# Kernel optimization log

Hardware: AMD Instinct MI355X
Metric: run time of the kernel (lower is better)

The kernel has to match this reference:

```python
import jax, jax.numpy as jnp
import numpy as np

LMAX, MMAX = 4, 2
L = (LMAX + 1) ** 2  # 25 full SH coefficients
_midx = np.concatenate([l * l + l + np.arange(-min(l, MMAX), min(l, MMAX) + 1) for l in range(LMAX + 1)])
M = len(_midx)  # 19 m-restricted coefficients (|m|<=mmax)
_l_of = np.concatenate([np.full(2 * l + 1, l) for l in range(LMAX + 1)])
MIDX = jnp.asarray(_midx)
L_OF = jnp.asarray(_l_of)
LMAP = jnp.asarray((_l_of[:, None] == np.arange(LMAX + 1)[None, :]).astype(np.float32))  # [L, lmax+1]
COUNTS = jnp.asarray((2 * np.arange(LMAX + 1) + 1).astype(np.float32))
AVG_DEGREE = 23.395238876342773
AVG_NUM_NODES = 77.81317
N_NODES, N_EDGES, N_GRAPH = 2500, 50000, 16
C, H, A, VC, FF, NB, NL = 128, 8, 64, 16, 128, 600, 4
MAX_R = 12.0

def rms_norm_sh(x, scale):
    # per-degree-l RMS norm with learned per-(l, channel) scale; x [N,L,C]
    ms = jnp.einsum('nlc,lk->nk', x * x, LMAP) / (COUNTS * x.shape[-1])
    inv = jax.lax.rsqrt(ms + 1e-8)[:, L_OF]  # [N,L]
    return x * inv[..., None] * scale[L_OF][None]

def seg_softmax(logits, seg, n):
    m = jax.ops.segment_max(logits, seg, num_segments=n)
    e = jnp.exp(logits - m[seg])
    s = jax.ops.segment_sum(e, seg, num_segments=n)
    return e / (s[seg] + 1e-9)

def _forward(edge_distance, sphere_emb, W_e1, W_e2, W_deg, norm_scale, norm_scale2,
             Wq, Wk, alpha_vec, Wv, W_rad, Wo, W1, W2, norm_scale_final, W_ef1, W_ef2,
             atomic_numbers, edge_index, batch):
    src, tgt = edge_index[0], edge_index[1]
    # GaussianSmearing(0, max_radius, 600, basis_width_scalar=2.0)
    offset = jnp.linspace(0.0, MAX_R, NB)
    coeff = -0.5 / (2.0 * (MAX_R / (NB - 1))) ** 2
    smear = jnp.exp(coeff * (edge_distance[:, None] - offset[None, :]) ** 2)  # [E,NB]
    efeat = jax.nn.silu(jax.nn.silu(smear @ W_e1) @ W_e2)  # shared radial edge features [E,C]
    # sphere embedding into l=0 coefficient
    x = jnp.zeros((N_NODES, L, C), edge_distance.dtype)
    x = x.at[:, 0, :].set(sphere_emb[atomic_numbers])
    # edge degree embedding: per-edge coefficients scattered to target nodes
    deg = (efeat @ W_deg).reshape(N_EDGES, M, C)
    x = x.at[:, MIDX, :].add(jax.ops.segment_sum(deg, tgt, num_segments=N_NODES) / AVG_DEGREE)
    for i in range(NL):
        # --- SO2 equivariant graph attention ---
        xn = rms_norm_sh(x, norm_scale[i])
        s = xn[:, 0, :]  # invariant (l=0) features [N,C]
        q = (s @ Wq[i]).reshape(N_NODES, H, A)[tgt]
        k = (s @ Wk[i]).reshape(N_NODES, H, A)[src]
        logits = jnp.einsum('eha,ha->eh', jax.nn.silu(q + k), alpha_vec[i]) / np.sqrt(A).astype(np.float32)
        attn = seg_softmax(logits, tgt, N_NODES)  # [E,H]
        rad = jax.nn.silu(efeat @ W_rad[i])  # per-edge per-coefficient radial gate [E,M]
        xm = xn[:, MIDX, :][src] * rad[..., None]  # gather m-restricted coeffs [E,M,C]
        v = jnp.einsum('emc,cd->emd', xm, Wv[i]).reshape(N_EDGES, M, H, VC)
        msg = (v * attn[:, None, :, None]).reshape(N_EDGES, M, H * VC)
        out = jnp.einsum('emd,dc->emc', msg, Wo[i])
        x = x.at[:, MIDX, :].add(jax.ops.segment_sum(out, tgt, num_segments=N_NODES))
        # --- FFN with separable S2 (scalar-gated) activation ---
        xn = rms_norm_sh(x, norm_scale2[i])
        h = jnp.einsum('nlc,cf->nlf', xn, W1[i])
        h = h * jax.nn.silu(h[:, :1, :])
        x = x + jnp.einsum('nlf,fc->nlc', h, W2[i])
    # energy head
    xn = rms_norm_sh(x, norm_scale_final)
    h = jnp.einsum('nlc,cf->nlf', xn, W_ef1)
    h = h * jax.nn.silu(h[:, :1, :])
    node_e = jnp.einsum('nlf,fo->nlo', h, W_ef2)[:, 0, 0]  # l=0 scalar per node
    return jax.ops.segment_sum(node_e, batch, num_segments=N_GRAPH) / AVG_NUM_NODES

def setup_inputs() -> dict:
    key = jax.random.key(0)
    ks = jax.random.split(key, 24)
    rn = lambda k, shp, fan: jax.random.normal(k, shp, jnp.float32) / np.sqrt(fan).astype(np.float32)
    inp = {}
    inp['atomic_numbers'] = jax.random.randint(ks[0], (N_NODES,), 0, 90)
    inp['edge_index'] = jax.random.randint(ks[1], (2, N_EDGES), 0, N_NODES)
    inp['edge_distance'] = jax.random.uniform(ks[2], (N_EDGES,), jnp.float32) * MAX_R
    inp['batch'] = jnp.sort(jax.random.randint(ks[3], (N_NODES,), 0, N_GRAPH))
    inp['sphere_emb'] = rn(ks[4], (90, C), 1)
    inp['W_e1'] = rn(ks[5], (NB, C), NB)
    inp['W_e2'] = rn(ks[6], (C, C), C)
    inp['W_deg'] = rn(ks[7], (C, M * C), C)
    inp['norm_scale'] = jnp.ones((NL, LMAX + 1, C), jnp.float32)
    inp['norm_scale2'] = jnp.ones((NL, LMAX + 1, C), jnp.float32)
    inp['Wq'] = rn(ks[8], (NL, C, H * A), C)
    inp['Wk'] = rn(ks[9], (NL, C, H * A), C)
    inp['alpha_vec'] = rn(ks[10], (NL, H, A), A)
    inp['Wv'] = rn(ks[11], (NL, C, H * VC), C)
    inp['W_rad'] = rn(ks[12], (NL, C, M), C)
    inp['Wo'] = rn(ks[13], (NL, H * VC, C), H * VC)
    inp['W1'] = rn(ks[14], (NL, C, FF), C)
    inp['W2'] = rn(ks[15], (NL, FF, C), FF)
    inp['norm_scale_final'] = jnp.ones((LMAX + 1, C), jnp.float32)
    inp['W_ef1'] = rn(ks[16], (C, FF), C)
    inp['W_ef2'] = rn(ks[17], (FF, 1), FF)
    return inp

def reference(atomic_numbers, edge_index, edge_distance, batch, sphere_emb, W_e1, W_e2, W_deg,
              norm_scale, norm_scale2, Wq, Wk, alpha_vec, Wv, W_rad, Wo, W1, W2,
              norm_scale_final, W_ef1, W_ef2):
    return _forward(edge_distance, sphere_emb, W_e1, W_e2, W_deg, norm_scale, norm_scale2,
                    Wq, Wk, alpha_vec, Wv, W_rad, Wo, W1, W2, norm_scale_final, W_ef1, W_ef2,
                    atomic_numbers, edge_index, batch)
```

## Files before the change

### kernel.cpp

```cpp
#include <hip/hip_runtime.h>
#include <hip/hip_bf16.h>

#define N_NODES 2500
#define N_EDGES 50000
#define C 128
#define MC 19
#define RSTR 20
#define NL 4
#define NB 600
#define GW 10
#define NTAP (2*GW+1)
#define NBUK 4
#define BUKW 625
#define N4 (N_NODES*NBUK)
#define ASTR 136
#define MSTR 132
#define MAXE 96
#define EB 64
#define NQKB ((N_NODES+31)/32)
#define NRADB ((N_EDGES+EB-1)/EB)

typedef float floatx2 __attribute__((ext_vector_type(2)));
typedef short bf16x8 __attribute__((ext_vector_type(8)));
typedef float f32x4 __attribute__((ext_vector_type(4)));
// ... 289 lines not shown
      float2 xv[MC];
      float pl[5]={0.f,0.f,0.f,0.f,0.f};
      #pragma unroll
      for (int m=0;m<MC;m++){
        float2 v = *(const float2*)&x[(size_t)n*MC*C + m*C + lane*2];
        xv[m]=v;
        pl[l_of_m(m)] += v.x*v.x + v.y*v.y;
      }
      #pragma unroll
      for (int l=0;l<5;l++){
        float r = pl[l];
        #pragma unroll
        for (int d=32; d>0; d>>=1) r += __shfl_xor(r, d, 64);
        pl[l]=r;
      }
      const float dens[5] = {128.f,384.f,640.f,896.f,1152.f};
      float inv[5];
      #pragma unroll
      for (int l=0;l<5;l++) inv[l] = 1.0f/sqrtf(pl[l]/dens[l] + 1e-8f);
      #pragma unroll
      for (int m=0;m<MC;m++){
        int l = l_of_m(m);
        float2 sc = *(const float2*)&scale0[l*C + lane*2];
        float a = xv[m].x*inv[l]*sc.x, b = xv[m].y*inv[l]*sc.y;
        *(unsigned*)&A16[(w*MC + m)*ASTR + lane*2] = pack2(a, b);
      }
    }
    for (int q=t; q<272; q+=256)
      ((unsigned*)A16)[(76*ASTR)/2 + q] = 0u;
    __syncthreads();
    int colb = 32*w;
    f32x4 acc[5][2];
    #pragma unroll
    for (int rt=0;rt<5;rt++)
      #pragma unroll
      for (int ci=0;ci<2;ci++){ acc[rt][ci][0]=0.f; acc[rt][ci][1]=0.f; acc[rt][ci][2]=0.f; acc[rt][ci][3]=0.f; }
    #pragma unroll
    for (int ks=0; ks<4; ++ks){
      int k0 = ks*32 + lg*8;
      const unsigned short* Ab = &A16[lr*ASTR + k0];
      bf16x8 a0 = *(const bf16x8*)(Ab);
      bf16x8 a1 = *(const bf16x8*)(Ab + 16*ASTR);
      bf16x8 a2 = *(const bf16x8*)(Ab + 32*ASTR);
      bf16x8 a3 = *(const bf16x8*)(Ab + 48*ASTR);
      bf16x8 a4 = *(const bf16x8*)(Ab + 64*ASTR);
      const unsigned short* Bb = &wvt[(colb + lr)*C + k0];
      bf16x8 b0 = *(const bf16x8*)(Bb);
      bf16x8 b1 = *(const bf16x8*)(Bb + 16*C);
      acc[0][0] = __builtin_amdgcn_mfma_f32_16x16x32_bf16(a0, b0, acc[0][0], 0, 0, 0);
      acc[1][0] = __builtin_amdgcn_mfma_f32_16x16x32_bf16(a1, b0, acc[1][0], 0, 0, 0);
      acc[2][0] = __builtin_amdgcn_mfma_f32_16x16x32_bf16(a2, b0, acc[2][0], 0, 0, 0);
      acc[3][0] = __builtin_amdgcn_mfma_f32_16x16x32_bf16(a3, b0, acc[3][0], 0, 0, 0);
      acc[4][0] = __builtin_amdgcn_mfma_f32_16x16x32_bf16(a4, b0, acc[4][0], 0, 0, 0);
      acc[0][1] = __builtin_amdgcn_mfma_f32_16x16x32_bf16(a0, b1, acc[0][1], 0, 0, 0);
      acc[1][1] = __builtin_amdgcn_mfma_f32_16x16x32_bf16(a1, b1, acc[1][1], 0, 0, 0);
      acc[2][1] = __builtin_amdgcn_mfma_f32_16x16x32_bf16(a2, b1, acc[2][1], 0, 0, 0);
      acc[3][1] = __builtin_amdgcn_mfma_f32_16x16x32_bf16(a3, b1, acc[3][1], 0, 0, 0);
      acc[4][1] = __builtin_amdgcn_mfma_f32_16x16x32_bf16(a4, b1, acc[4][1], 0, 0, 0);
    }
    __syncthreads();
    #pragma unroll
    for (int rt=0;rt<5;rt++){
      #pragma unroll
      for (int ci=0;ci<2;ci++){
        int col = colb + 16*ci + lr;
        #pragma unroll
        for (int q=0;q<4;q++){
          int r = 16*rt + lg*4 + q;
          A16[r*ASTR + col] = bf16of(acc[rt][ci][q]);
        }
      }
    }
    __syncthreads();
    for (int q=t; q<76*64; q+=256){
      int r = q>>6;
      int c2 = (q&63)*2;
      unsigned u = *(unsigned*)&A16[r*ASTR + c2];
      float2 f = bf2f2(u);
      *(unsigned short*)&V[((size_t)(n0*MC + r))*C + c2] = packfp8(f.x, f.y);
    }
  } else {
    int qq = blockIdx.x - N_NODES/4;
    int grp = qq / NQKB;
    int n0 = (qq - grp*NQKB)*32;
    float (*sn)[132] = (float(*)[132])smem;
    float (*ps)[8] = (float(*)[8])(smem + 16896);
    float* invs = (float*)(smem + 16896 + 1024);
    unsigned short* A16 = (unsigned short*)(smem + 16896 + 1024 + 128);
    const unsigned short* WTg = (grp < 4) ? wqt : wkt;
    int cb = (grp & 3)*128;
    unsigned short* outb = (grp < 4) ? qb : kb;
    {
      int nd = t>>3, seg = t&7;
      int n = n0+nd;
      float ss = 0.f;
      if (n < N_NODES){
        const float* xr = &x[(size_t)n*MC*C];
        #pragma unroll
        for (int i=0;i<16;i++){
          int c = seg*16+i;
          float v = xr[c];
          ss += v*v;
          sn[nd][c] = v*scale0[c];
        }
      } else {
        #pragma unroll
        for (int i=0;i<16;i++) sn[nd][seg*16+i] = 0.f;
      }
      ps[nd][seg] = ss;
    }
    __syncthreads();
    if (t < 32){
      float s = 0.f;
      #pragma unroll
      for (int i=0;i<8;i++) s += ps[t][i];
      invs[t] = 1.0f/sqrtf(s*(1.0f/128.f) + 1e-8f);
    }
    __syncthreads();
    for (int q=t; q<32*64; q+=256){
      int r = q>>6, c2 = (q&63)*2;
      float inv = invs[r];
      *(unsigned*)&A16[r*ASTR + c2] = pack2(sn[r][c2]*inv, sn[r][c2+1]*inv);
    }
    __syncthreads();
    int colb = 32*w;
    f32x4 acc[2][2];
    #pragma unroll
    for (int rt=0;rt<2;rt++)
      #pragma unroll
      for (int ci=0;ci<2;ci++){ acc[rt][ci][0]=0.f; acc[rt][ci][1]=0.f; acc[rt][ci][2]=0.f; acc[rt][ci][3]=0.f; }
    #pragma unroll
    for (int ks=0; ks<4; ++ks){
      int k0 = ks*32 + lg*8;
      const unsigned short* Ab = &A16[lr*ASTR + k0];
      bf16x8 a0 = *(const bf16x8*)(Ab);
      bf16x8 a1 = *(const bf16x8*)(Ab + 16*ASTR);
      const unsigned short* Bb = &WTg[(size_t)(cb + colb + lr)*C + k0];
      bf16x8 b0 = *(const bf16x8*)(Bb);
      bf16x8 b1 = *(const bf16x8*)(Bb + 16*C);
      acc[0][0] = __builtin_amdgcn_mfma_f32_16x16x32_bf16(a0, b0, acc[0][0], 0, 0, 0);
      acc[1][0] = __builtin_amdgcn_mfma_f32_16x16x32_bf16(a1, b0, acc[1][0], 0, 0, 0);
      acc[0][1] = __builtin_amdgcn_mfma_f32_16x16x32_bf16(a0, b1, acc[0][1], 0, 0, 0);
      acc[1][1] = __builtin_amdgcn_mfma_f32_16x16x32_bf16(a1, b1, acc[1][1], 0, 0, 0);
    }
    #pragma unroll
    for (int rt=0;rt<2;rt++){
      #pragma unroll
      for (int ci=0;ci<2;ci++){
        int col = colb + 16*ci + lr;
        #pragma unroll
        for (int q=0;q<4;q++){
          int r = 16*rt + lg*4 + q;
          int n = n0 + r;
          if (n < N_NODES)
            outb[(size_t)n*512 + cb + col] = bf16of(acc[rt][ci][q]);
        }
      }
    }
  }
}

__global__ __launch_bounds__(256) void k_attnrad(const unsigned short* __restrict__ qb,
        const unsigned short* __restrict__ kb, const float* __restrict__ alpha,
        const int* __restrict__ rowptr, const int2* __restrict__ epair, float* __restrict__ attnb,
        const unsigned short* __restrict__ efeat16, const float* __restrict__ Wrad,
        float* __restrict__ radb){
  __shared__ __align__(16) char smem[13824];
  int t = threadIdx.x;
  int w = t>>6, lane = t&63;
  if (blockIdx.x < (unsigned)(N_NODES/4)){
    float (*lw)[MAXE][8] = (float(*)[MAXE][8])smem;
    int (*eid)[MAXE] = (int(*)[MAXE])(smem + 12288);
    int n = blockIdx.x*4 + w;
    float al[8];
    {
      float4 a0 = *(const float4*)&alpha[lane*8];
      float4 a1 = *(const float4*)&alpha[lane*8+4];
      al[0]=a0.x; al[1]=a0.y; al[2]=a0.z; al[3]=a0.w;
      al[4]=a1.x; al[5]=a1.y; al[6]=a1.z; al[7]=a1.w;
    }
    float qf[8];
    {
      int4 qv = *(const int4*)&qb[(size_t)n*512 + lane*8];
      unsigned qu[4] = {(unsigned)qv.x,(unsigned)qv.y,(unsigned)qv.z,(unsigned)qv.w};
      #pragma unroll
      for (int j=0;j<4;j++){
        float2 q2 = bf2f2(qu[j]);
        qf[2*j] = q2.x; qf[2*j+1] = q2.y;
      }
    }
    int beg = rowptr[n*NBUK], end = rowptr[n*NBUK+NBUK];
    int cnt = end - beg; if (cnt > MAXE) cnt = MAXE;
    int i = 0;
    for (; i+2 <= cnt; i += 2){
      int2 p0 = epair[beg+i];
      int2 p1 = epair[beg+i+1];
      int4 kv0 = *(const int4*)&kb[(size_t)p0.y*512 + lane*8];
      int4 kv1 = *(const int4*)&kb[(size_t)p1.y*512 + lane*8];
      unsigned ku0[4] = {(unsigned)kv0.x,(unsigned)kv0.y,(unsigned)kv0.z,(unsigned)kv0.w};
      unsigned ku1[4] = {(unsigned)kv1.x,(unsigned)kv1.y,(unsigned)kv1.z,(unsigned)kv1.w};
      float acc0 = 0.f, acc1 = 0.f;
      #pragma unroll
      for (int j=0;j<4;j++){
        float2 k0 = bf2f2(ku0[j]);
        float2 k1 = bf2f2(ku1[j]);
        acc0 += silu(qf[2*j]+k0.x)*al[2*j] + silu(qf[2*j+1]+k0.y)*al[2*j+1];
        acc1 += silu(qf[2*j]+k1.x)*al[2*j] + silu(qf[2*j+1]+k1.y)*al[2*j+1];
      }
      #pragma unroll
      for (int d=1; d<8; d<<=1){
        acc0 += __shfl_down(acc0, d, 64);
        acc1 += __shfl_down(acc1, d, 64);
      }
      if ((lane&7)==0){
        lw[w][i][lane>>3]   = acc0 * 0.125f;
        lw[w][i+1][lane>>3] = acc1 * 0.125f;
      }
      if (lane==0){ eid[w][i] = p0.x; eid[w][i+1] = p1.x; }
    }
    for (; i < cnt; ++i){
      int2 p0 = epair[beg+i];
      int4 kv0 = *(const int4*)&kb[(size_t)p0.y*512 + lane*8];
      unsigned ku0[4] = {(unsigned)kv0.x,(unsigned)kv0.y,(unsigned)kv0.z,(unsigned)kv0.w};
      float acc0 = 0.f;
      #pragma unroll
      for (int j=0;j<4;j++){
        float2 k0 = bf2f2(ku0[j]);
        acc0 += silu(qf[2*j]+k0.x)*al[2*j] + silu(qf[2*j+1]+k0.y)*al[2*j+1];
      }
      #pragma unroll
      for (int d=1; d<8; d<<=1) acc0 += __shfl_down(acc0, d, 64);
      if ((lane&7)==0) lw[w][i][lane>>3] = acc0 * 0.125f;
      if (lane==0) eid[w][i] = p0.x;
    }
    __syncthreads();
    int h = lane & 7, ec = lane >> 3;
    float mx = -1e30f;
    for (int q=ec; q<cnt; q+=8) mx = fmaxf(mx, lw[w][q][h]);
    #pragma unroll
    for (int dd=8; dd<64; dd<<=1) mx = fmaxf(mx, __shfl_xor(mx, dd, 64));
    float sum = 0.f;
    for (int q=ec; q<cnt; q+=8) sum += __expf(lw[w][q][h] - mx);
    #pragma unroll
    for (int dd=8; dd<64; dd<<=1) sum += __shfl_xor(sum, dd, 64);
    float inv = 1.0f/(sum + 1e-9f);
    for (int q=ec; q<cnt; q+=8)
      attnb[eid[w][q]*8 + h] = __expf(lw[w][q][h] - mx) * inv;
  } else {
    unsigned short* WT = (unsigned short*)smem;
    int e0 = (blockIdx.x - N_NODES/4)*EB;
    for (int q=t; q<32*64; q+=256){
      int m = q>>6, c2 = (q&63)*2;
      float w0 = (m < MC) ? Wrad[(size_t)c2*MC + m] : 0.f;
      float w1 = (m < MC) ? Wrad[(size_t)(c2+1)*MC + m] : 0.f;
      *(unsigned*)&WT[m*ASTR + c2] = pack2(w0, w1);
    }
    __syncthreads();
    int lr = lane & 15, lg = lane >> 4;
    f32x4 acc[2];
    acc[0][0]=0.f; acc[0][1]=0.f; acc[0][2]=0.f; acc[0][3]=0.f;
    acc[1][0]=0.f; acc[1][1]=0.f; acc[1][2]=0.f; acc[1][3]=0.f;
    const unsigned short* Ag = &efeat16[(size_t)(e0 + 16*w + lr)*C];
    #pragma unroll
    for (int ks=0; ks<4; ++ks){
      int k0 = ks*32 + lg*8;
      bf16x8 a  = *(const bf16x8*)(Ag + k0);
      bf16x8 b0 = *(const bf16x8*)&WT[lr*ASTR + k0];
      bf16x8 b1 = *(const bf16x8*)&WT[(16+lr)*ASTR + k0];
      acc[0] = __builtin_amdgcn_mfma_f32_16x16x32_bf16(a, b0, acc[0], 0, 0, 0);
      acc[1] = __builtin_amdgcn_mfma_f32_16x16x32_bf16(a, b1, acc[1], 0, 0, 0);
    }
    #pragma unroll
    for (int ci=0;ci<2;ci++){
      int m = 16*ci + lr;
      #pragma unroll
      for (int q=0;q<4;q++){
        int r = 16*w + lg*4 + q;
        int e = e0 + r;
        if (m < MC && e < N_EDGES)
          radb[(size_t)e*RSTR + m] = silu(acc[ci][q]);
      }
    }
  }
}

#define CONS1(vv, ar)  { \
    floatx2 g0 = __builtin_amdgcn_cvt_pk_f32_fp8((vv).x, false); \
    floatx2 g1 = __builtin_amdgcn_cvt_pk_f32_fp8((vv).x, true);  \
    floatx2 g2 = __builtin_amdgcn_cvt_pk_f32_fp8((vv).y, false); \
    floatx2 g3 = __builtin_amdgcn_cvt_pk_f32_fp8((vv).y, true);  \
    acc1[0] += (ar)*g0[0]; acc1[1] += (ar)*g0[1]; \
    acc1[2] += (ar)*g1[0]; acc1[3] += (ar)*g1[1]; \
    acc1[4] += (ar)*g2[0]; acc1[5] += (ar)*g2[1]; \
    acc1[6] += (ar)*g3[0]; acc1[7] += (ar)*g3[1]; }
#define CONS2(vv, ar)  { \
    floatx2 g0 = __builtin_amdgcn_cvt_pk_f32_fp8((vv).x, false); \
    floatx2 g1 = __builtin_amdgcn_cvt_pk_f32_fp8((vv).x, true);  \
    floatx2 g2 = __builtin_amdgcn_cvt_pk_f32_fp8((vv).y, false); \
    floatx2 g3 = __builtin_amdgcn_cvt_pk_f32_fp8((vv).y, true);  \
    acc2[0] += (ar)*g0[0]; acc2[1] += (ar)*g0[1]; \
    acc2[2] += (ar)*g1[0]; acc2[3] += (ar)*g1[1]; \
    acc2[4] += (ar)*g2[0]; acc2[5] += (ar)*g2[1]; \
    acc2[6] += (ar)*g3[0]; acc2[7] += (ar)*g3[1]; }
__global__ __launch_bounds__(256, 4) void k_e1(const unsigned char* __restrict__ V, const float* __restrict__ radb,
        const float* __restrict__ attnb, const unsigned short* __restrict__ wot,
        const int* __restrict__ rowptr, const int2* __restrict__ epair,
        float* __restrict__ x){
  __shared__ __align__(16) float msum[32*MSTR];
  int n = blockIdx.x;
  int t = threadIdx.x;
  int w = t>>6, lane = t&63;
  for (int q=t; q<13*MSTR; q+=256) msum[19*MSTR + q] = 0.f;
  int chunk = lane & 15;
  int g = lane >> 4;
  int m1 = w*5 + g;
  int c1 = chunk*8;
  int h1 = chunk>>1;
  int m2 = w*5 + 4;
  bool has2 = (w < 3) && (lane < 16);
  int voff1 = m1*C + c1;
  int voff2 = m2*C + lane*8;
  int h2 = lane>>1;
  float acc1[8], acc2[8];
  #pragma unroll
  for (int j=0;j<8;j++){ acc1[j]=0.f; acc2[j]=0.f; }
  int beg = rowptr[n*NBUK], end = rowptr[n*NBUK+NBUK];
  int idx = beg;
  for (; idx+4 <= end; idx += 4){
    int2 p0 = epair[idx];
    int2 p1 = epair[idx+1];
    int2 p2 = epair[idx+2];
    int2 p3 = epair[idx+3];
    const unsigned char* vb0 = V + (size_t)p0.y*(MC*C);
    const unsigned char* vb1 = V + (size_t)p1.y*(MC*C);
    const unsigned char* vb2 = V + (size_t)p2.y*(MC*C);
    const unsigned char* vb3 = V + (size_t)p3.y*(MC*C);
    int2 va0 = *(const int2*)(vb0 + voff1);
    int2 va1 = *(const int2*)(vb1 + voff1);
    int2 va2 = *(const int2*)(vb2 + voff1);
    int2 va3 = *(const int2*)(vb3 + voff1);
    float ra0 = attnb[p0.x*8 + h1] * radb[(size_t)p0.x*RSTR + m1];
    float ra1 = attnb[p1.x*8 + h1] * radb[(size_t)p1.x*RSTR + m1];
    float ra2 = attnb[p2.x*8 + h1] * radb[(size_t)p2.x*RSTR + m1];
    float ra3 = attnb[p3.x*8 + h1] * radb[(size_t)p3.x*RSTR + m1];
    int2 wa0, wa1, wa2, wa3;
    float qa0=0.f, qa1=0.f, qa2=0.f, qa3=0.f;
    if (has2){
      wa0 = *(const int2*)(vb0 + voff2);
      wa1 = *(const int2*)(vb1 + voff2);
      wa2 = *(const int2*)(vb2 + voff2);
      wa3 = *(const int2*)(vb3 + voff2);
      qa0 = attnb[p0.x*8 + h2] * radb[(size_t)p0.x*RSTR + m2];
      qa1 = attnb[p1.x*8 + h2] * radb[(size_t)p1.x*RSTR + m2];
      qa2 = attnb[p2.x*8 + h2] * radb[(size_t)p2.x*RSTR + m2];
      qa3 = attnb[p3.x*8 + h2] * radb[(size_t)p3.x*RSTR + m2];
    }
    CONS1(va0, ra0);
    CONS1(va1, ra1);
    CONS1(va2, ra2);
    CONS1(va3, ra3);
    if (has2){
      CONS2(wa0, qa0);
      CONS2(wa1, qa1);
      CONS2(wa2, qa2);
      CONS2(wa3, qa3);
    }
  }
  for (; idx < end; ++idx){
    int2 p0 = epair[idx];
    const unsigned char* vb = V + (size_t)p0.y*(MC*C);
    int2 va = *(const int2*)(vb + voff1);
    float ra = attnb[p0.x*8 + h1] * radb[(size_t)p0.x*RSTR + m1];
    int2 wa; float qa = 0.f;
    if (has2){
      wa = *(const int2*)(vb + voff2);
      qa = attnb[p0.x*8 + h2] * radb[(size_t)p0.x*RSTR + m2];
    }
    CONS1(va, ra);
    if (has2){ CONS2(wa, qa); }
  }
  {
    float4 st0; st0.x=acc1[0]; st0.y=acc1[1]; st0.z=acc1[2]; st0.w=acc1[3];
    float4 st1; st1.x=acc1[4]; st1.y=acc1[5]; st1.z=acc1[6]; st1.w=acc1[7];
    *(float4*)&msum[m1*MSTR + c1]     = st0;
    *(float4*)&msum[m1*MSTR + c1 + 4] = st1;
    if (has2){
      float4 s2a; s2a.x=acc2[0]; s2a.y=acc2[1]; s2a.z=acc2[2]; s2a.w=acc2[3];
      float4 s2b; s2b.x=acc2[4]; s2b.y=acc2[5]; s2b.z=acc2[6]; s2b.w=acc2[7];
      *(float4*)&msum[m2*MSTR + lane*8]     = s2a;
      *(float4*)&msum[m2*MSTR + lane*8 + 4] = s2b;
    }
  }
  __syncthreads();
  int lr = lane & 15, lg = lane >> 4;
  int colb = 32*w;
  f32x4 eacc[2][2];
  #pragma unroll
  for (int rt=0;rt<2;rt++)
    #pragma unroll
    for (int ci=0;ci<2;ci++){ eacc[rt][ci][0]=0.f; eacc[rt][ci][1]=0.f; eacc[rt][ci][2]=0.f; eacc[rt][ci][3]=0.f; }
  #pragma unroll
  for (int ks=0; ks<4; ++ks){
    int k0 = ks*32 + lg*8;
    float4 a0lo = *(const float4*)&msum[lr*MSTR + k0];
    float4 a0hi = *(const float4*)&msum[lr*MSTR + k0 + 4];
    float4 a1lo = *(const float4*)&msum[(lr+16)*MSTR + k0];
    float4 a1hi = *(const float4*)&msum[(lr+16)*MSTR + k0 + 4];
    bf16x8 a0 = packbf8(a0lo, a0hi);
    bf16x8 a1 = packbf8(a1lo, a1hi);
    const unsigned short* Bb = &wot[(colb + lr)*C + k0];
    bf16x8 b0 = *(const bf16x8*)(Bb);
    bf16x8 b1 = *(const bf16x8*)(Bb + 16*C);
    eacc[0][0] = __builtin_amdgcn_mfma_f32_16x16x32_bf16(a0, b0, eacc[0][0], 0, 0, 0);
    eacc[1][0] = __builtin_amdgcn_mfma_f32_16x16x32_bf16(a1, b0, eacc[1][0], 0, 0, 0);
    eacc[0][1] = __builtin_amdgcn_mfma_f32_16x16x32_bf16(a0, b1, eacc[0][1], 0, 0, 0);
    eacc[1][1] = __builtin_amdgcn_mfma_f32_16x16x32_bf16(a1, b1, eacc[1][1], 0, 0, 0);
  }
  #pragma unroll
  for (int rt=0;rt<2;rt++){
    #pragma unroll
    for (int ci=0;ci<2;ci++){
      int col = colb + 16*ci + lr;
      #pragma unroll
      for (int q=0;q<4;q++){
        int r = 16*rt + lg*4 + q;
        if (r < MC){
          size_t off = (size_t)n*MC*C + r*C + col;
          x[off] += eacc[rt][ci][q];
        }
      }
    }
  }
}

__global__ __launch_bounds__(256) void k_nodeB(float* __restrict__ x, const float* __restrict__ scale,
        const unsigned short* __restrict__ w1t, const unsigned short* __restrict__ w2t){
  __shared__ __align__(16) unsigned short A16[80*ASTR];
  __shared__ float gate[4*C];
  int t = threadIdx.x;
  int n0 = blockIdx.x*4;
  int w = t>>6, lane = t&63;
  int lr = lane & 15, lg = lane >> 4;
  {
    int n = n0 + w;
    float2 xv[MC];
    float pl[5]={0.f,0.f,0.f,0.f,0.f};
    #pragma unroll
    for (int m=0;m<MC;m++){
      float2 v = *(const float2*)&x[(size_t)n*MC*C + m*C + lane*2];
      xv[m]=v;
      pl[l_of_m(m)] += v.x*v.x + v.y*v.y;
    }
    #pragma unroll
    for (int l=0;l<5;l++){
      float r = pl[l];
      #pragma unroll
      for (int d=32; d>0; d>>=1) r += __shfl_xor(r, d, 64);
      pl[l]=r;
    }
    const float dens[5] = {128.f,384.f,640.f,896.f,1152.f};
    float inv[5];
    #pragma unroll
    for (int l=0;l<5;l++) inv[l] = 1.0f/sqrtf(pl[l]/dens[l] + 1e-8f);
    #pragma unroll
    for (int m=0;m<MC;m++){
      int l = l_of_m(m);
      float2 sc = *(const float2*)&scale[l*C + lane*2];
      float a = xv[m].x*inv[l]*sc.x, b = xv[m].y*inv[l]*sc.y;
      *(unsigned*)&A16[(w*MC + m)*ASTR + lane*2] = pack2(a, b);
    }
  }
  for (int q=t; q<272; q+=256)
    ((unsigned*)A16)[(76*ASTR)/2 + q] = 0u;
  __syncthreads();
  int colb = 32*w;
  f32x4 acc[5][2];
  #pragma unroll
  for (int rt=0;rt<5;rt++)
    #pragma unroll
    for (int ci=0;ci<2;ci++){ acc[rt][ci][0]=0.f; acc[rt][ci][1]=0.f; acc[rt][ci][2]=0.f; acc[rt][ci][3]=0.f; }
  #pragma unroll
  for (int ks=0; ks<4; ++ks){
    int k0 = ks*32 + lg*8;
    const unsigned short* Ab = &A16[lr*ASTR + k0];
    bf16x8 a0 = *(const bf16x8*)(Ab);
    bf16x8 a1 = *(const bf16x8*)(Ab + 16*ASTR);
    bf16x8 a2 = *(const bf16x8*)(Ab + 32*ASTR);
    bf16x8 a3 = *(const bf16x8*)(Ab + 48*ASTR);
    bf16x8 a4 = *(const bf16x8*)(Ab + 64*ASTR);
    const unsigned short* Bb = &w1t[(colb + lr)*C + k0];
    bf16x8 b0 = *(const bf16x8*)(Bb);
    bf16x8 b1 = *(const bf16x8*)(Bb + 16*C);
    acc[0][0] = __builtin_amdgcn_mfma_f32_16x16x32_bf16(a0, b0, acc[0][0], 0, 0, 0);
    acc[1][0] = __builtin_amdgcn_mfma_f32_16x16x32_bf16(a1, b0, acc[1][0], 0, 0, 0);
    acc[2][0] = __builtin_amdgcn_mfma_f32_16x16x32_bf16(a2, b0, acc[2][0], 0, 0, 0);
    acc[3][0] = __builtin_amdgcn_mfma_f32_16x16x32_bf16(a3, b0, acc[3][0], 0, 0, 0);
    acc[4][0] = __builtin_amdgcn_mfma_f32_16x16x32_bf16(a4, b0, acc[4][0], 0, 0, 0);
    acc[0][1] = __builtin_amdgcn_mfma_f32_16x16x32_bf16(a0, b1, acc[0][1], 0, 0, 0);
    acc[1][1] = __builtin_amdgcn_mfma_f32_16x16x32_bf16(a1, b1, acc[1][1], 0, 0, 0);
    acc[2][1] = __builtin_amdgcn_mfma_f32_16x16x32_bf16(a2, b1, acc[2][1], 0, 0, 0);
    acc[3][1] = __builtin_amdgcn_mfma_f32_16x16x32_bf16(a3, b1, acc[3][1], 0, 0, 0);
    acc[4][1] = __builtin_amdgcn_mfma_f32_16x16x32_bf16(a4, b1, acc[4][1], 0, 0, 0);
  }
  __syncthreads();
  #pragma unroll
  for (int rt=0;rt<5;rt++){
    #pragma unroll
    for (int ci=0;ci<2;ci++){
      int col = colb + 16*ci + lr;
      #pragma unroll
      for (int q=0;q<4;q++){
        int r = 16*rt + lg*4 + q;
        A16[r*ASTR + col] = bf16of(acc[rt][ci][q]);
      }
    }
  }
  __syncthreads();
  #pragma unroll
  for (int i=0;i<2;++i){
    int id = t + (i<<8);
    int j = id>>7, c = id&127;
    float v = __uint_as_float(((unsigned)A16[(j*MC)*ASTR + c]) << 16);
    gate[j*C + c] = silu(v);
  }
  __syncthreads();
  for (int q=t; q<76*64; q+=256){
    int r = q>>6;
    int c2 = (q&63)*2;
    int j = r/MC;
    unsigned u = *(unsigned*)&A16[r*ASTR + c2];
    float2 f = bf2f2(u);
    f.x *= gate[j*C + c2];
    f.y *= gate[j*C + c2 + 1];
    *(unsigned*)&A16[r*ASTR + c2] = pack2(f.x, f.y);
  }
  __syncthreads();
  #pragma unroll
  for (int rt=0;rt<5;rt++)
    #pragma unroll
    for (int ci=0;ci<2;ci++){ acc[rt][ci][0]=0.f; acc[rt][ci][1]=0.f; acc[rt][ci][2]=0.f; acc[rt][ci][3]=0.f; }
  #pragma unroll
  for (int ks=0; ks<4; ++ks){
    int k0 = ks*32 + lg*8;
    const unsigned short* Ab = &A16[lr*ASTR + k0];
    bf16x8 a0 = *(const bf16x8*)(Ab);
    bf16x8 a1 = *(const bf16x8*)(Ab + 16*ASTR);
    bf16x8 a2 = *(const bf16x8*)(Ab + 32*ASTR);
    bf16x8 a3 = *(const bf16x8*)(Ab + 48*ASTR);
    bf16x8 a4 = *(const bf16x8*)(Ab + 64*ASTR);
    const unsigned short* Bb = &w2t[(colb + lr)*C + k0];
    bf16x8 b0 = *(const bf16x8*)(Bb);
    bf16x8 b1 = *(const bf16x8*)(Bb + 16*C);
    acc[0][0] = __builtin_amdgcn_mfma_f32_16x16x32_bf16(a0, b0, acc[0][0], 0, 0, 0);
    acc[1][0] = __builtin_amdgcn_mfma_f32_16x16x32_bf16(a1, b0, acc[1][0], 0, 0, 0);
    acc[2][0] = __builtin_amdgcn_mfma_f32_16x16x32_bf16(a2, b0, acc[2][0], 0, 0, 0);
    acc[3][0] = __builtin_amdgcn_mfma_f32_16x16x32_bf16(a3, b0, acc[3][0], 0, 0, 0);
    acc[4][0] = __builtin_amdgcn_mfma_f32_16x16x32_bf16(a4, b0, acc[4][0], 0, 0, 0);
    acc[0][1] = __builtin_amdgcn_mfma_f32_16x16x32_bf16(a0, b1, acc[0][1], 0, 0, 0);
    acc[1][1] = __builtin_amdgcn_mfma_f32_16x16x32_bf16(a1, b1, acc[1][1], 0, 0, 0);
    acc[2][1] = __builtin_amdgcn_mfma_f32_16x16x32_bf16(a2, b1, acc[2][1], 0, 0, 0);
    acc[3][1] = __builtin_amdgcn_mfma_f32_16x16x32_bf16(a3, b1, acc[3][1], 0, 0, 0);
    acc[4][1] = __builtin_amdgcn_mfma_f32_16x16x32_bf16(a4, b1, acc[4][1], 0, 0, 0);
  }
  #pragma unroll
  for (int rt=0;rt<5;rt++){
    #pragma unroll
    for (int ci=0;ci<2;ci++){
      int col = colb + 16*ci + lr;
      #pragma unroll
      for (int q=0;q<4;q++){
        int r = 16*rt + lg*4 + q;
        if (r < 4*MC){
          size_t off = ((size_t)(n0*MC + r))*C + col;
          x[off] += acc[rt][ci][q];
        }
      }
    }
  }
}

__global__ __launch_bounds__(128) void k_final(const float* x, const float* nsf, const float* Wef1,
        const float* Wef2, const int* batch, float* out){
  __shared__ float sl[C];
  __shared__ float red[2];
  __shared__ float red2[2];
  int n = blockIdx.x; int t = threadIdx.x;
  float v = x[(size_t)n*MC*C + t];
  float sq = v*v;
  for (int d=32; d>0; d>>=1) sq += __shfl_down(sq, d, 64);
  if ((t&63)==0) red[t>>6] = sq;
  __syncthreads();
  float ms = (red[0]+red[1]) * (1.0f/128.f);
  float inv = 1.0f/sqrtf(ms + 1e-8f);
  sl[t] = v*inv*nsf[t];
  __syncthreads();
  float acc = 0.f;
  for (int cc=0; cc<C; ++cc) acc += sl[cc]*Wef1[cc*C + t];
  float val = acc*silu(acc)*Wef2[t];
  for (int d=32; d>0; d>>=1) val += __shfl_down(val, d, 64);
  if ((t&63)==0) red2[t>>6] = val;
  __syncthreads();
  if (t==0){
    float ne = red2[0]+red2[1];
    atomicAdd(&out[batch[n]], ne * (1.0f/77.81317f));
  }
}

extern "C" void kernel_launch(void* const* d_in, const int* in_sizes, int n_in,
                              void* d_out, int out_size, void* d_ws, size_t ws_size,
                              hipStream_t stream){
  (void)in_sizes; (void)n_in; (void)ws_size;
  const int*   anum  = (const int*)d_in[0];
  const int*   eidx  = (const int*)d_in[1];
  const float* dist  = (const float*)d_in[2];
  const int*   batch = (const int*)d_in[3];
  const float* emb   = (const float*)d_in[4];
  const float* We1   = (const float*)d_in[5];
  const float* We2   = (const float*)d_in[6];
  const float* Wdeg  = (const float*)d_in[7];
  const float* ns1   = (const float*)d_in[8];
  const float* ns2   = (const float*)d_in[9];
  const float* Wq    = (const float*)d_in[10];
  const float* Wk    = (const float*)d_in[11];
  const float* alpha = (const float*)d_in[12];
  const float* Wv    = (const float*)d_in[13];
  const float* Wrad  = (const float*)d_in[14];
  const float* Wo    = (const float*)d_in[15];
  const float* W1    = (const float*)d_in[16];
  const float* W2    = (const float*)d_in[17];
  const float* nsf   = (const float*)d_in[18];
  const float* Wef1  = (const float*)d_in[19];
  const float* Wef2  = (const float*)d_in[20];
  float* out = (float*)d_out;

  const int* srcarr = eidx;
  const int* tgtarr = eidx + N_EDGES;

  char* wsb = (char*)d_ws;
  unsigned short* efeat16 = (unsigned short*)wsb; wsb += (size_t)(NRADB*EB)*C*2;
  float* efsumT= (float*)wsb;  wsb += (size_t)N_NODES*C*4;
  float* x     = (float*)wsb;  wsb += (size_t)N_NODES*MC*C*4;
  unsigned char* Vb = (unsigned char*)wsb; wsb += (size_t)N_NODES*MC*C;
  unsigned short* qb = (unsigned short*)wsb; wsb += (size_t)N_NODES*512*2;
  unsigned short* kb = (unsigned short*)wsb; wsb += (size_t)N_NODES*512*2;
  float* attnb = (float*)wsb;  wsb += (size_t)N_EDGES*8*4;
  float* radb  = (float*)wsb;  wsb += (size_t)N_EDGES*RSTR*4;
  int* deg     = (int*)wsb;    wsb += (size_t)N4*4;
  int* rowptr  = (int*)wsb;    wsb += (size_t)(N4+1)*4;
  int* cursor  = (int*)wsb;    wsb += (size_t)N4*4;
  int* elist   = (int*)wsb;    wsb += (size_t)N_EDGES*4;
  int2* epair  = (int2*)wsb;   wsb += (size_t)N_EDGES*8;
  unsigned short* we2t = (unsigned short*)wsb; wsb += (size_t)16384*2;
  unsigned short* wvt  = (unsigned short*)wsb; wsb += (size_t)4*16384*2;
  unsigned short* wot  = (unsigned short*)wsb; wsb += (size_t)4*16384*2;
  unsigned short* w1t  = (unsigned short*)wsb; wsb += (size_t)4*16384*2;
  unsigned short* w2t  = (unsigned short*)wsb; wsb += (size_t)4*16384*2;
  unsigned short* wqt  = (unsigned short*)wsb; wsb += (size_t)4*65536*2;
  unsigned short* wkt  = (unsigned short*)wsb; wsb += (size_t)4*65536*2;

  (void)hipMemsetAsync(deg, 0, N4*4, stream);
  (void)hipMemsetAsync(cursor, 0, N4*4, stream);
  (void)hipMemsetAsync(d_out, 0, (size_t)out_size*sizeof(float), stream);

  k_packall<<<1568, 256, 0, stream>>>(We2, Wv, Wo, W1, W2, Wq, Wk,
                                      we2t, wvt, wot, w1t, w2t, wqt, wkt);
  k_count<<<(N_EDGES+255)/256, 256, 0, stream>>>(tgtarr, srcarr, deg);
  k_scan<<<1, 1024, 0, stream>>>(deg, rowptr);
  k_fill<<<(N_EDGES+255)/256, 256, 0, stream>>>(tgtarr, srcarr, rowptr, cursor, elist, epair);
  k_efeat<<<NRADB, 256, 0, stream>>>(dist, We1, we2t, efeat16);
  k_efsum<<<N_NODES, 128, 0, stream>>>(efeat16, rowptr, elist, efsumT);
  k_deginit<<<dim3((N_NODES+15)/16, 5), 256, 0, stream>>>(efsumT, Wdeg, emb, anum, x);

  for (int i=0;i<NL;i++){
    k_nAqk<<<N_NODES/4 + NQKB*8, 256, 0, stream>>>(x, ns1 + i*5*C,
                                                   wvt + (size_t)i*16384,
                                                   wqt + (size_t)i*65536, wkt + (size_t)i*65536,
                                                   Vb, qb, kb);
    k_attnrad<<<N_NODES/4 + NRADB, 256, 0, stream>>>(qb, kb, alpha + i*512, rowptr, epair, attnb,
                                                     efeat16, Wrad + i*C*MC, radb);
    k_e1<<<N_NODES, 256, 0, stream>>>(Vb, radb, attnb, wot + (size_t)i*16384,
                                      rowptr, epair, x);
    k_nodeB<<<N_NODES/4, 256, 0, stream>>>(x, ns2 + i*5*C, w1t + (size_t)i*16384, w2t + (size_t)i*16384);
  }
  k_final<<<N_NODES, 128, 0, stream>>>(x, nsf, Wef1, Wef2, batch, out);
}
```

Before: 640.3 us.

## Fuse node FFN block into per-node edge aggregation kernel

Merges k_nodeB (RMS norm, gated W1/W2 FFN) into the tail of k_e1, so each per-node block keeps the updated x rows in shared memory and runs the FFN at once. This drops one launch per layer and a global read of x. In exchange the FFN MFMAs now process one node (19 rows padded to 32) per block instead of four nodes (76 rows padded to 80), which wastes more matrix work. The fused kernel also uses more shared memory, which may lower occupancy.

```diff
diff --git a/kernel.cpp b/kernel.cpp
--- a/kernel.cpp
+++ b/kernel.cpp
@@ -615,11 +615,16 @@
     acc2[2] += (ar)*g1[0]; acc2[3] += (ar)*g1[1]; \
     acc2[4] += (ar)*g2[0]; acc2[5] += (ar)*g2[1]; \
     acc2[6] += (ar)*g3[0]; acc2[7] += (ar)*g3[1]; }
-__global__ __launch_bounds__(256, 4) void k_e1(const unsigned char* __restrict__ V, const float* __restrict__ radb,
+__global__ __launch_bounds__(256, 4) void k_e1nB(const unsigned char* __restrict__ V, const float* __restrict__ radb,
         const float* __restrict__ attnb, const unsigned short* __restrict__ wot,
         const int* __restrict__ rowptr, const int2* __restrict__ epair,
+        const float* __restrict__ scale2,
+        const unsigned short* __restrict__ w1t, const unsigned short* __restrict__ w2t,
         float* __restrict__ x){
   __shared__ __align__(16) float msum[32*MSTR];
+  __shared__ __align__(16) unsigned short A16[32*ASTR];
+  __shared__ float gate[C];
+  __shared__ float ssum[5];
   int n = blockIdx.x;
   int t = threadIdx.x;
   int w = t>>6, lane = t&63;
@@ -729,6 +734,8 @@
     eacc[0][1] = __builtin_amdgcn_mfma_f32_16x16x32_bf16(a0, b1, eacc[0][1], 0, 0, 0);
     eacc[1][1] = __builtin_amdgcn_mfma_f32_16x16x32_bf16(a1, b1, eacc[1][1], 0, 0, 0);
   }
+  __syncthreads();
+  if (t < 5) ssum[t] = 0.f;
   #pragma unroll
   for (int rt=0;rt<2;rt++){
     #pragma unroll
@@ -739,153 +746,123 @@
         int r = 16*rt + lg*4 + q;
         if (r < MC){
           size_t off = (size_t)n*MC*C + r*C + col;
-          x[off] += eacc[rt][ci][q];
+          float xn = x[off] + eacc[rt][ci][q];
+          x[off] = xn;
+          msum[r*MSTR + col] = xn;
         }
       }
     }
   }
-}
-
-__global__ __launch_bounds__(256) void k_nodeB(float* __restrict__ x, const float* __restrict__ scale,
-        const unsigned short* __restrict__ w1t, const unsigned short* __restrict__ w2t){
-  __shared__ __align__(16) unsigned short A16[80*ASTR];
-  __shared__ float gate[4*C];
-  int t = threadIdx.x;
-  int n0 = blockIdx.x*4;
-  int w = t>>6, lane = t&63;
-  int lr = lane & 15, lg = lane >> 4;
-  {
-    int n = n0 + w;
-    float2 xv[MC];
+  __syncthreads();
+  float vals[MC];
+  float invl[5];
+  if (t < 128){
+    int c = t;
     float pl[5]={0.f,0.f,0.f,0.f,0.f};
     #pragma unroll
     for (int m=0;m<MC;m++){
-      float2 v = *(const float2*)&x[(size_t)n*MC*C + m*C + lane*2];
-      xv[m]=v;
-      pl[l_of_m(m)] += v.x*v.x + v.y*v.y;
+      float v = msum[m*MSTR + c];
+      vals[m]=v;
+      pl[l_of_m(m)] += v*v;
     }
     #pragma unroll
     for (int l=0;l<5;l++){
       float r = pl[l];
       #pragma unroll
-      for (int d=32; d>0; d>>=1) r += __shfl_xor(r, d, 64);
-      pl[l]=r;
-    }
+      for (int d=32; d>0; d>>=1) r += __shfl_down(r, d, 64);
+      if ((t&63)==0) atomicAdd(&ssum[l], r);
+    }
+  }
+  __syncthreads();
+  {
     const float dens[5] = {128.f,384.f,640.f,896.f,1152.f};
-    float inv[5];
-    #pragma unroll
-    for (int l=0;l<5;l++) inv[l] = 1.0f/sqrtf(pl[l]/dens[l] + 1e-8f);
+    #pragma unroll
+    for (int l=0;l<5;l++) invl[l] = 1.0f/sqrtf(ssum[l]/dens[l] + 1e-8f);
+  }
+  if (t < 128){
+    int c = t;
     #pragma unroll
     for (int m=0;m<MC;m++){
       int l = l_of_m(m);
-      float2 sc = *(const float2*)&scale[l*C + lane*2];
-      float a = xv[m].x*inv[l]*sc.x, b = xv[m].y*inv[l]*sc.y;
-      *(unsigned*)&A16[(w*MC + m)*ASTR + lane*2] = pack2(a, b);
-    }
-  }
-  for (int q=t; q<272; q+=256)
-    ((unsigned*)A16)[(76*ASTR)/2 + q] = 0u;
-  __syncthreads();
-  int colb = 32*w;
-  f32x4 acc[5][2];
-  #pragma unroll
-  for (int rt=0;rt<5;rt++)
-    #pragma unroll
-    for (int ci=0;ci<2;ci++){ acc[rt][ci][0]=0.f; acc[rt][ci][1]=0.f; acc[rt][ci][2]=0.f; acc[rt][ci][3]=0.f; }
+      A16[m*ASTR + c] = bf16of(vals[m]*invl[l]*scale2[l*C + c]);
+    }
+  }
+  for (int q=t; q<884; q+=256)
+    ((unsigned*)A16)[(19*ASTR)/2 + q] = 0u;
+  __syncthreads();
+  f32x4 facc[2][2];
+  #pragma unroll
+  for (int rt=0;rt<2;rt++)
+    #pragma unroll
+    for (int ci=0;ci<2;ci++){ facc[rt][ci][0]=0.f; facc[rt][ci][1]=0.f; facc[rt][ci][2]=0.f; facc[rt][ci][3]=0.f; }
   #pragma unroll
   for (int ks=0; ks<4; ++ks){
     int k0 = ks*32 + lg*8;
-    const unsigned short* Ab = &A16[lr*ASTR + k0];
-    bf16x8 a0 = *(const bf16x8*)(Ab);
-    bf16x8 a1 = *(const bf16x8*)(Ab + 16*ASTR);
-    bf16x8 a2 = *(const bf16x8*)(Ab + 32*ASTR);
-    bf16x8 a3 = *(const bf16x8*)(Ab + 48*ASTR);
-    bf16x8 a4 = *(const bf16x8*)(Ab + 64*ASTR);
+    bf16x8 a0 = *(const bf16x8*)&A16[lr*ASTR + k0];
+    bf16x8 a1 = *(const bf16x8*)&A16[(lr+16)*ASTR + k0];
     const unsigned short* Bb = &w1t[(colb + lr)*C + k0];
     bf16x8 b0 = *(const bf16x8*)(Bb);
     bf16x8 b1 = *(const bf16x8*)(Bb + 16*C);
-    acc[0][0] = __builtin_amdgcn_mfma_f32_16x16x32_bf16(a0, b0, acc[0][0], 0, 0, 0);
-    acc[1][0] = __builtin_amdgcn_mfma_f32_16x16x32_bf16(a1, b0, acc[1][0], 0, 0, 0);
-    acc[2][0] = __builtin_amdgcn_mfma_f32_16x16x32_bf16(a2, b0, acc[2][0], 0, 0, 0);
-    acc[3][0] = __builtin_amdgcn_mfma_f32_16x16x32_bf16(a3, b0, acc[3][0], 0, 0, 0);
-    acc[4][0] = __builtin_amdgcn_mfma_f32_16x16x32_bf16(a4, b0, acc[4][0], 0, 0, 0);
-    acc[0][1] = __builtin_amdgcn_mfma_f32_16x16x32_bf16(a0, b1, acc[0][1], 0, 0, 0);
-    acc[1][1] = __builtin_amdgcn_mfma_f32_16x16x32_bf16(a1, b1, acc[1][1], 0, 0, 0);
-    acc[2][1] = __builtin_amdgcn_mfma_f32_16x16x32_bf16(a2, b1, acc[2][1], 0, 0, 0);
-    acc[3][1] = __builtin_amdgcn_mfma_f32_16x16x32_bf16(a3, b1, acc[3][1], 0, 0, 0);
-    acc[4][1] = __builtin_amdgcn_mfma_f32_16x16x32_bf16(a4, b1, acc[4][1], 0, 0, 0);
-  }
-  __syncthreads();
-  #pragma unroll
-  for (int rt=0;rt<5;rt++){
+    facc[0][0] = __builtin_amdgcn_mfma_f32_16x16x32_bf16(a0, b0, facc[0][0], 0, 0, 0);
+    facc[1][0] = __builtin_amdgcn_mfma_f32_16x16x32_bf16(a1, b0, facc[1][0], 0, 0, 0);
+    facc[0][1] = __builtin_amdgcn_mfma_f32_16x16x32_bf16(a0, b1, facc[0][1], 0, 0, 0);
+    facc[1][1] = __builtin_amdgcn_mfma_f32_16x16x32_bf16(a1, b1, facc[1][1], 0, 0, 0);
+  }
+  __syncthreads();
+  #pragma unroll
+  for (int rt=0;rt<2;rt++){
     #pragma unroll
     for (int ci=0;ci<2;ci++){
       int col = colb + 16*ci + lr;
       #pragma unroll
       for (int q=0;q<4;q++){
         int r = 16*rt + lg*4 + q;
-        A16[r*ASTR + col] = bf16of(acc[rt][ci][q]);
-      }
-    }
-  }
-  __syncthreads();
-  #pragma unroll
-  for (int i=0;i<2;++i){
-    int id = t + (i<<8);
-    int j = id>>7, c = id&127;
-    float v = __uint_as_float(((unsigned)A16[(j*MC)*ASTR + c]) << 16);
-    gate[j*C + c] = silu(v);
-  }
-  __syncthreads();
-  for (int q=t; q<76*64; q+=256){
+        A16[r*ASTR + col] = (r < MC) ? bf16of(facc[rt][ci][q]) : (unsigned short)0;
+      }
+    }
+  }
+  __syncthreads();
+  if (t < 128)
+    gate[t] = silu(bf2f(A16[t]));
+  __syncthreads();
+  for (int q=t; q<19*64; q+=256){
     int r = q>>6;
     int c2 = (q&63)*2;
-    int j = r/MC;
     unsigned u = *(unsigned*)&A16[r*ASTR + c2];
     float2 f = bf2f2(u);
-    f.x *= gate[j*C + c2];
-    f.y *= gate[j*C + c2 + 1];
+    f.x *= gate[c2];
+    f.y *= gate[c2+1];
     *(unsigned*)&A16[r*ASTR + c2] = pack2(f.x, f.y);
   }
   __syncthreads();
   #pragma unroll
-  for (int rt=0;rt<5;rt++)
-    #pragma unroll
-    for (int ci=0;ci<2;ci++){ acc[rt][ci][0]=0.f; acc[rt][ci][1]=0.f; acc[rt][ci][2]=0.f; acc[rt][ci][3]=0.f; }
+  for (int rt=0;rt<2;rt++)
+    #pragma unroll
+    for (int ci=0;ci<2;ci++){ facc[rt][ci][0]=0.f; facc[rt][ci][1]=0.f; facc[rt][ci][2]=0.f; facc[rt][ci][3]=0.f; }
   #pragma unroll
   for (int ks=0; ks<4; ++ks){
     int k0 = ks*32 + lg*8;
-    const unsigned short* Ab = &A16[lr*ASTR + k0];
-    bf16x8 a0 = *(const bf16x8*)(Ab);
-    bf16x8 a1 = *(const bf16x8*)(Ab + 16*ASTR);
-    bf16x8 a2 = *(const bf16x8*)(Ab + 32*ASTR);
-    bf16x8 a3 = *(const bf16x8*)(Ab + 48*ASTR);
-    bf16x8 a4 = *(const bf16x8*)(Ab + 64*ASTR);
+    bf16x8 a0 = *(const bf16x8*)&A16[lr*ASTR + k0];
+    bf16x8 a1 = *(const bf16x8*)&A16[(lr+16)*ASTR + k0];
     const unsigned short* Bb = &w2t[(colb + lr)*C + k0];
     bf16x8 b0 = *(const bf16x8*)(Bb);
     bf16x8 b1 = *(const bf16x8*)(Bb + 16*C);
-    acc[0][0] = __builtin_amdgcn_mfma_f32_16x16x32_bf16(a0, b0, acc[0][0], 0, 0, 0);
-    acc[1][0] = __builtin_amdgcn_mfma_f32_16x16x32_bf16(a1, b0, acc[1][0], 0, 0, 0);
-    acc[2][0] = __builtin_amdgcn_mfma_f32_16x16x32_bf16(a2, b0, acc[2][0], 0, 0, 0);
-    acc[3][0] = __builtin_amdgcn_mfma_f32_16x16x32_bf16(a3, b0, acc[3][0], 0, 0, 0);
-    acc[4][0] = __builtin_amdgcn_mfma_f32_16x16x32_bf16(a4, b0, acc[4][0], 0, 0, 0);
-    acc[0][1] = __builtin_amdgcn_mfma_f32_16x16x32_bf16(a0, b1, acc[0][1], 0, 0, 0);
-    acc[1][1] = __builtin_amdgcn_mfma_f32_16x16x32_bf16(a1, b1, acc[1][1], 0, 0, 0);
-    acc[2][1] = __builtin_amdgcn_mfma_f32_16x16x32_bf16(a2, b1, acc[2][1], 0, 0, 0);
-    acc[3][1] = __builtin_amdgcn_mfma_f32_16x16x32_bf16(a3, b1, acc[3][1], 0, 0, 0);
-    acc[4][1] = __builtin_amdgcn_mfma_f32_16x16x32_bf16(a4, b1, acc[4][1], 0, 0, 0);
-  }
-  #pragma unroll
-  for (int rt=0;rt<5;rt++){
+    facc[0][0] = __builtin_amdgcn_mfma_f32_16x16x32_bf16(a0, b0, facc[0][0], 0, 0, 0);
+    facc[1][0] = __builtin_amdgcn_mfma_f32_16x16x32_bf16(a1, b0, facc[1][0], 0, 0, 0);
+    facc[0][1] = __builtin_amdgcn_mfma_f32_16x16x32_bf16(a0, b1, facc[0][1], 0, 0, 0);
+    facc[1][1] = __builtin_amdgcn_mfma_f32_16x16x32_bf16(a1, b1, facc[1][1], 0, 0, 0);
+  }
+  #pragma unroll
+  for (int rt=0;rt<2;rt++){
     #pragma unroll
     for (int ci=0;ci<2;ci++){
       int col = colb + 16*ci + lr;
       #pragma unroll
       for (int q=0;q<4;q++){
         int r = 16*rt + lg*4 + q;
-        if (r < 4*MC){
-          size_t off = ((size_t)(n0*MC + r))*C + col;
-          x[off] += acc[rt][ci][q];
+        if (r < MC){
+          size_t off = (size_t)n*MC*C + r*C + col;
+          x[off] += facc[rt][ci][q];
         }
       }
     }
@@ -991,9 +968,9 @@
                                                    Vb, qb, kb);
     k_attnrad<<<N_NODES/4 + NRADB, 256, 0, stream>>>(qb, kb, alpha + i*512, rowptr, epair, attnb,
                                                      efeat16, Wrad + i*C*MC, radb);
-    k_e1<<<N_NODES, 256, 0, stream>>>(Vb, radb, attnb, wot + (size_t)i*16384,
-                                      rowptr, epair, x);
-    k_nodeB<<<N_NODES/4, 256, 0, stream>>>(x, ns2 + i*5*C, w1t + (size_t)i*16384, w2t + (size_t)i*16384);
+    k_e1nB<<<N_NODES, 256, 0, stream>>>(Vb, radb, attnb, wot + (size_t)i*16384,
+                                        rowptr, epair, ns2 + i*5*C,
+                                        w1t + (size_t)i*16384, w2t + (size_t)i*16384, x);
   }
   k_final<<<N_NODES, 128, 0, stream>>>(x, nsf, Wef1, Wef2, batch, out);
 }
```

After: 694.7 us. 8.5% more time.
